# Optimization experiments

Hardware: AMD Instinct MI355X
Metric: run time of the kernel (lower is better)

## Reference

```python
import jax, jax.numpy as jnp
import numpy as np

D = 256; NH = 8; NL = 4; NP = 4; DFF = 2048; HD = D // NH
SHAPES = [(64, 64), (32, 32), (16, 16), (8, 8)]
B = 2; LEN = sum(h * w for h, w in SHAPES)


def setup_inputs() -> dict:
    key = jax.random.key(0)
    ks = jax.random.split(key, 12)
    def w(k, shape, s=0.02):
        return jax.random.normal(k, shape, jnp.float32) * s
    starts = np.cumsum([0] + [h * w for h, w in SHAPES[:-1]])
    return {
        "src": jax.random.normal(ks[0], (B, LEN, D), jnp.float32),
        "pos": jax.random.normal(ks[1], (B, LEN, D), jnp.float32) * 0.1,
        "spatial_shapes": jnp.array(SHAPES, dtype=jnp.int32),
        "level_start_index": jnp.array(starts, dtype=jnp.int32),
        "w_value": w(ks[2], (D, D)), "b_value": jnp.zeros((D,), jnp.float32),
        "w_off": w(ks[3], (D, NH * NL * NP * 2)), "b_off": w(ks[4], (NH * NL * NP * 2,), 0.1),
        "w_attn": w(ks[5], (D, NH * NL * NP)), "b_attn": jnp.zeros((NH * NL * NP,), jnp.float32),
        "w_out": w(ks[6], (D, D)), "b_out": jnp.zeros((D,), jnp.float32),
        "w1": w(ks[7], (D, DFF)), "b1": jnp.zeros((DFF,), jnp.float32),
        "w2": w(ks[8], (DFF, D)), "b2": jnp.zeros((D,), jnp.float32),
        "g1": jnp.ones((D,), jnp.float32), "be1": jnp.zeros((D,), jnp.float32),
        "g2": jnp.ones((D,), jnp.float32), "be2": jnp.zeros((D,), jnp.float32),
    }


def _layer_norm(x, g, b):
    mu = jnp.mean(x, -1, keepdims=True)
    v = jnp.var(x, -1, keepdims=True)
    return (x - mu) * jax.lax.rsqrt(v + 1e-5) * g + b


def _reference_points(shapes):
    # torch.linspace(0.5, H-0.5, H)/H == (arange(H)+0.5)/H
    refs = []
    for H, W in shapes:
        ry = (jnp.arange(H, dtype=jnp.float32) + 0.5) / H
        rx = (jnp.arange(W, dtype=jnp.float32) + 0.5) / W
        yy, xx = jnp.meshgrid(ry, rx, indexing='ij')
        refs.append(jnp.stack([xx.ravel(), yy.ravel()], -1))
    return jnp.concatenate(refs, 0)  # (Len, 2) as (x, y)


def _ms_deform_sample(value, loc, shapes):
    # value: (B, Len, NH, HD); loc: (B, Lq, NH, NL, NP, 2) normalized [0,1]
    # Replicates torch grid_sample(bilinear, padding='zeros', align_corners=False).
    Bn, Lq = loc.shape[0], loc.shape[1]
    P = loc.shape[4]
    start = 0
    outs = []
    for lvl, (H, W) in enumerate(shapes):
        v = value[:, start:start + H * W].transpose(0, 2, 1, 3)  # (B, NH, HW, HD)
        start += H * W
        l = loc[:, :, :, lvl]                      # (B, Lq, NH, P, 2)
        x = l[..., 0] * W - 0.5
        y = l[..., 1] * H - 0.5
        x0 = jnp.floor(x); y0 = jnp.floor(y)
        dx = x - x0; dy = y - y0
        x0i = x0.astype(jnp.int32); y0i = y0.astype(jnp.int32)
        acc = None
        for xi, yi, wgt in ((x0i, y0i, (1 - dx) * (1 - dy)),
                            (x0i + 1, y0i, dx * (1 - dy)),
                            (x0i, y0i + 1, (1 - dx) * dy),
                            (x0i + 1, y0i + 1, dx * dy)):
            valid = ((xi >= 0) & (xi < W) & (yi >= 0) & (yi < H)).astype(value.dtype)
            idx = jnp.clip(yi, 0, H - 1) * W + jnp.clip(xi, 0, W - 1)  # (B, Lq, NH, P)
            idx = idx.transpose(0, 2, 1, 3).reshape(Bn, NH, Lq * P)
            g = jnp.take_along_axis(v, idx[..., None], axis=2).reshape(Bn, NH, Lq, P, HD)
            w = (wgt * valid).transpose(0, 2, 1, 3)[..., None]  # (B, NH, Lq, P, 1)
            acc = g * w if acc is None else acc + g * w
        outs.append(acc)  # (B, NH, Lq, P, HD)
    return jnp.stack(outs, 3)  # (B, NH, Lq, NL, NP, HD)


def _forward(src, pos, w_value, b_value, w_off, b_off, w_attn, b_attn,
             w_out, b_out, w1, b1, w2, b2, g1, be1, g2, be2, shapes):
    Bn, Lq, _ = src.shape
    q = src + pos  # with_pos_embed
    value = (src @ w_value + b_value).reshape(Bn, Lq, NH, HD)
    off = (q @ w_off + b_off).reshape(Bn, Lq, NH, NL, NP, 2)
    attn = jax.nn.softmax((q @ w_attn + b_attn).reshape(Bn, Lq, NH, NL * NP), -1)
    attn = attn.reshape(Bn, Lq, NH, NL, NP)
    ref = _reference_points(shapes)  # (Len, 2)
    normalizer = jnp.array([[w_, h_] for h_, w_ in shapes], jnp.float32)  # (NL, 2) = (W, H)
    loc = ref[None, :, None, None, None, :] + off / normalizer[None, None, None, :, None, :]
    sampled = _ms_deform_sample(value, loc, shapes)  # (B, NH, Lq, NL, NP, HD)
    out = jnp.einsum('bqhlp,bhqlpd->bqhd', attn, sampled).reshape(Bn, Lq, D)
    out = out @ w_out + b_out
    x = _layer_norm(src + out, g1, be1)           # residual + norm1
    ff = jax.nn.relu(x @ w1 + b1) @ w2 + b2       # FFN (dropout=0)
    return _layer_norm(x + ff, g2, be2)           # residual + norm2


def reference(src, pos, spatial_shapes, level_start_index, w_value, b_value,
              w_off, b_off, w_attn, b_attn, w_out, b_out, w1, b1, w2, b2,
              g1, be1, g2, be2):
    shapes = [tuple(int(v) for v in s) for s in np.asarray(spatial_shapes)]
    return _forward(src, pos, w_value, b_value, w_off, b_off, w_attn, b_attn,
                    w_out, b_out, w1, b1, w2, b2, g1, be1, g2, be2, shapes)
```

## Files before the change

kernel.cpp:

```cpp
#include <hip/hip_runtime.h>
#include <math.h>

#define D 256
#define NH 8
#define NL 4
#define NP 4
#define DFF 2048
#define HD 32
#define BB 2
#define LEN 5440
#define MROWS (BB * LEN)

typedef __attribute__((ext_vector_type(8))) short short8;
typedef __attribute__((ext_vector_type(4))) float f32x4;
typedef unsigned int uint32;

__device__ __forceinline__ unsigned short f2bf(float f) {
    uint32 u = __float_as_uint(f);
    u += 0x7FFF + ((u >> 16) & 1);
    return (unsigned short)(u >> 16);
}
__device__ __forceinline__ float bf2f(unsigned short h) {
    return __uint_as_float(((uint32)h) << 16);
}
__device__ __forceinline__ uint32 pack2(float a, float b) {
    return (uint32)f2bf(a) | ((uint32)f2bf(b) << 16);
}

__device__ __forceinline__ void swz85(int b, int ncols, int& row, int& col) {
    const int gsz = ncols << 3;
    const int full = 10 * gsz;
    if (b < full) {
        const int g = b / gsz, idx = b - g * gsz;
        row = (g << 3) + (idx & 7);
        col = idx >> 3;
    } else {
        const int idx = b - full;
        row = 80 + idx % 5;
        col = idx / 5;
    }
}

__global__ void prep(const float* __restrict__ w_value, const float* __restrict__ w_off,
                     const float* __restrict__ w_attn, const float* __restrict__ w_out,
                     const float* __restrict__ w1, const float* __restrict__ w2,
                     const float* __restrict__ b_value, const float* __restrict__ b_off,
                     const float* __restrict__ b_attn,
                     unsigned short* __restrict__ wqvT, unsigned short* __restrict__ woT,
                     unsigned short* __restrict__ w1T, unsigned short* __restrict__ w2T,
                     float* __restrict__ bqv) {
    const int blk = blockIdx.x;
    if (blk >= 1248) {
        for (int i = threadIdx.x; i < 640; i += 256)
            bqv[i] = (i < 256) ? b_value[i] : (i < 512 ? b_off[i - 256] : b_attn[i - 512]);
        return;
    }
    const float* W; unsigned short* WT; int K, N, tid;
    if (blk < 64)       { W = w_value; WT = wqvT;             K = 256;  N = 256;  tid = blk; }
    else if (blk < 128) { W = w_off;   WT = wqvT + 256 * 256; K = 256;  N = 256;  tid = blk - 64; }
    else if (blk < 160) { W = w_attn;  WT = wqvT + 512 * 256; K = 256;  N = 128;  tid = blk - 128; }
    else if (blk < 224) { W = w_out;   WT = woT;              K = 256;  N = 256;  tid = blk - 160; }
    else if (blk < 736) { W = w1;      WT = w1T;              K = 256;  N = 2048; tid = blk - 224; }
    else                { W = w2;      WT = w2T;              K = 2048; N = 256;  tid = blk - 736; }
    const int ntx = N >> 5;
    const int nb = (tid % ntx) * 32, kb = (tid / ntx) * 32;

    __shared__ float tile[32][33];
    const int tx = threadIdx.x & 31, ty = threadIdx.x >> 5;
#pragma unroll
    for (int i = 0; i < 32; i += 8)
        tile[ty + i][tx] = W[(size_t)(kb + ty + i) * N + nb + tx];
    __syncthreads();
#pragma unroll
    for (int i = 0; i < 32; i += 8)
        WT[(size_t)(nb + ty + i) * K + kb + tx] = f2bf(tile[tx][ty + i]);
}

__global__ __launch_bounds__(256) void ffn1_gemm(
        const unsigned short* __restrict__ A,
        const unsigned short* __restrict__ BT, const float* __restrict__ bias,
        unsigned short* __restrict__ Cv, int N, int K, int lda, int ldb) {
    __shared__ unsigned short Ash[2][128][40];
    __shared__ unsigned short Bsh[2][128][40];

    int rowt, colt;
    swz85(blockIdx.x, N >> 7, rowt, colt);
    const int row0 = rowt * 128, col0 = colt * 128;

    const int t = threadIdx.x;
    const int wave = t >> 6, lane = t & 63;
    const int wr = wave >> 1, wc = wave & 1;
    const int lrow = lane & 15, quad = lane >> 4;
    const int srow = t >> 1;
    const int cb = (t & 1) * 16;

    const unsigned short* ap = A + (size_t)(row0 + srow) * lda + cb;
    const unsigned short* bp = BT + (size_t)(col0 + srow) * ldb + cb;

    f32x4 acc[4][4];
#pragma unroll
    for (int i = 0; i < 4; i++)
#pragma unroll
        for (int j = 0; j < 4; j++) acc[i][j] = (f32x4){0.f, 0.f, 0.f, 0.f};

    uint4 ra0 = *(const uint4*)(ap + 0), ra1 = *(const uint4*)(ap + 8);
    uint4 rb0 = *(const uint4*)(bp + 0), rb1 = *(const uint4*)(bp + 8);
    *(uint4*)&Ash[0][srow][cb + 0] = ra0;
    *(uint4*)&Ash[0][srow][cb + 8] = ra1;
    *(uint4*)&Bsh[0][srow][cb + 0] = rb0;
    *(uint4*)&Bsh[0][srow][cb + 8] = rb1;
    if (32 < K) {
        ra0 = *(const uint4*)(ap + 32); ra1 = *(const uint4*)(ap + 40);
        rb0 = *(const uint4*)(bp + 32); rb1 = *(const uint4*)(bp + 40);
    }

    int i = 0;
    for (int kb = 0; kb < K; kb += 32, ++i) {
        __syncthreads();
        if (kb + 32 < K) {
            const int nb = (i + 1) & 1;
            *(uint4*)&Ash[nb][srow][cb + 0] = ra0;
            *(uint4*)&Ash[nb][srow][cb + 8] = ra1;
            *(uint4*)&Bsh[nb][srow][cb + 0] = rb0;
            *(uint4*)&Bsh[nb][srow][cb + 8] = rb1;
            if (kb + 64 < K) {
                ra0 = *(const uint4*)(ap + kb + 64 + 0);
                ra1 = *(const uint4*)(ap + kb + 64 + 8);
                rb0 = *(const uint4*)(bp + kb + 64 + 0);
                rb1 = *(const uint4*)(bp + kb + 64 + 8);
            }
        }
        const int cf = i & 1;
        short8 af[4], bfr[4];
#pragma unroll
        for (int mt = 0; mt < 4; mt++)
            af[mt] = *(const short8*)&Ash[cf][wr * 64 + mt * 16 + lrow][quad * 8];
#pragma unroll
        for (int nt = 0; nt < 4; nt++)
            bfr[nt] = *(const short8*)&Bsh[cf][wc * 64 + nt * 16 + lrow][quad * 8];
#pragma unroll
        for (int mt = 0; mt < 4; mt++)
#pragma unroll
            for (int nt = 0; nt < 4; nt++)
                acc[mt][nt] = __builtin_amdgcn_mfma_f32_16x16x32_bf16(
                    af[mt], bfr[nt], acc[mt][nt], 0, 0, 0);
    }

#pragma unroll
    for (int nt = 0; nt < 4; nt++) {
        const int col = col0 + wc * 64 + nt * 16 + lrow;
        const float bv = bias[col];
#pragma unroll
        for (int mt = 0; mt < 4; mt++) {
            f32x4 a = acc[mt][nt];
#pragma unroll
            for (int r = 0; r < 4; r++) {
                const int row = row0 + wr * 64 + mt * 16 + quad * 4 + r;
                Cv[(size_t)row * N + col] = f2bf(fmaxf(a[r] + bv, 0.f));
            }
        }
    }
}

template <int NZ>
__global__ __launch_bounds__(256) void splitk_gemm(
        const unsigned short* __restrict__ A, const unsigned short* __restrict__ BT,
        unsigned short* __restrict__ part, int KC, int lda, int ldb) {
    __shared__ unsigned short Ash[2][128][40];
    __shared__ unsigned short Bsh[2][128][40];

    int rowt, cc;
    swz85(blockIdx.x, 2 * NZ, rowt, cc);
    const int row0 = rowt * 128;
    const int col0 = (cc & 1) * 128;
    const int z = cc >> 1;
    const int koff = z * KC;
    unsigned short* __restrict__ C = part + (size_t)z * MROWS * 256;

    const int t = threadIdx.x;
    const int wave = t >> 6, lane = t & 63;
    const int wr = wave >> 1, wc = wave & 1;
    const int lrow = lane & 15, quad = lane >> 4;
    const int srow = t >> 1;
    const int cb = (t & 1) * 16;

    const unsigned short* ap = A + (size_t)(row0 + srow) * lda + koff + cb;
    const unsigned short* bp = BT + (size_t)(col0 + srow) * ldb + koff + cb;

    f32x4 acc[4][4];
#pragma unroll
    for (int i = 0; i < 4; i++)
#pragma unroll
        for (int j = 0; j < 4; j++) acc[i][j] = (f32x4){0.f, 0.f, 0.f, 0.f};

    uint4 ra0 = *(const uint4*)(ap + 0), ra1 = *(const uint4*)(ap + 8);
    uint4 rb0 = *(const uint4*)(bp + 0), rb1 = *(const uint4*)(bp + 8);
    *(uint4*)&Ash[0][srow][cb + 0] = ra0;
    *(uint4*)&Ash[0][srow][cb + 8] = ra1;
    *(uint4*)&Bsh[0][srow][cb + 0] = rb0;
    *(uint4*)&Bsh[0][srow][cb + 8] = rb1;
    if (32 < KC) {
        ra0 = *(const uint4*)(ap + 32); ra1 = *(const uint4*)(ap + 40);
        rb0 = *(const uint4*)(bp + 32); rb1 = *(const uint4*)(bp + 40);
    }

    int i = 0;
    for (int kb = 0; kb < KC; kb += 32, ++i) {
        __syncthreads();
        if (kb + 32 < KC) {
            const int nb = (i + 1) & 1;
            *(uint4*)&Ash[nb][srow][cb + 0] = ra0;
            *(uint4*)&Ash[nb][srow][cb + 8] = ra1;
            *(uint4*)&Bsh[nb][srow][cb + 0] = rb0;
            *(uint4*)&Bsh[nb][srow][cb + 8] = rb1;
            if (kb + 64 < KC) {
                ra0 = *(const uint4*)(ap + kb + 64 + 0);
                ra1 = *(const uint4*)(ap + kb + 64 + 8);
                rb0 = *(const uint4*)(bp + kb + 64 + 0);
                rb1 = *(const uint4*)(bp + kb + 64 + 8);
            }
        }
        const int cf = i & 1;
        short8 af[4], bfr[4];
#pragma unroll
        for (int mt = 0; mt < 4; mt++)
            af[mt] = *(const short8*)&Ash[cf][wr * 64 + mt * 16 + lrow][quad * 8];
#pragma unroll
        for (int nt = 0; nt < 4; nt++)
            bfr[nt] = *(const short8*)&Bsh[cf][wc * 64 + nt * 16 + lrow][quad * 8];
#pragma unroll
        for (int mt = 0; mt < 4; mt++)
#pragma unroll
            for (int nt = 0; nt < 4; nt++)
                acc[mt][nt] = __builtin_amdgcn_mfma_f32_16x16x32_bf16(
                    af[mt], bfr[nt], acc[mt][nt], 0, 0, 0);
    }

#pragma unroll
    for (int nt = 0; nt < 4; nt++) {
        const int col = col0 + wc * 64 + nt * 16 + lrow;
#pragma unroll
        for (int mt = 0; mt < 4; mt++) {
            f32x4 a = acc[mt][nt];
#pragma unroll
            for (int r = 0; r < 4; r++) {
                const int row = row0 + wr * 64 + mt * 16 + quad * 4 + r;
                C[(size_t)row * 256 + col] = f2bf(a[r]);
            }
        }
    }
}

__global__ __launch_bounds__(256) void gemm_ln(
        const unsigned short* __restrict__ A, const unsigned short* __restrict__ BT,
        const float* __restrict__ bias, const float* __restrict__ rsd,
        const float* __restrict__ g, const float* __restrict__ be,
        unsigned short* __restrict__ out16, int K) {
    __shared__ __align__(16) unsigned short Ash[32][40];
    __shared__ __align__(16) unsigned short Bsh[256][40];
    __shared__ float red1[4][32], red2[4][32];

    const int row0 = blockIdx.x * 32;
    const int t = threadIdx.x;
    const int wave = t >> 6, lane = t & 63;
    const int lrow = lane & 15, quad = lane >> 4;

    const int ar = t >> 3, ac = (t & 7) * 4;
    const unsigned short* ap = A + (size_t)(row0 + ar) * K + ac;
    const int br = t >> 1, cb = (t & 1) * 16;
    const unsigned short* bp0 = BT + (size_t)br * K + cb;
    const unsigned short* bp1 = BT + (size_t)(128 + br) * K + cb;

    f32x4 acc[2][4];
#pragma unroll
    for (int i = 0; i < 2; i++)
#pragma unroll
        for (int j = 0; j < 4; j++) acc[i][j] = (f32x4){0.f, 0.f, 0.f, 0.f};

    uint2 ra = *(const uint2*)ap;
    uint4 rb00 = *(const uint4*)(bp0 + 0), rb01 = *(const uint4*)(bp0 + 8);
    uint4 rb10 = *(const uint4*)(bp1 + 0), rb11 = *(const uint4*)(bp1 + 8);

    for (int kb = 0; kb < K; kb += 32) {
        __syncthreads();
        *(uint2*)&Ash[ar][ac] = ra;
        *(uint4*)&Bsh[br][cb + 0] = rb00;
        *(uint4*)&Bsh[br][cb + 8] = rb01;
        *(uint4*)&Bsh[128 + br][cb + 0] = rb10;
        *(uint4*)&Bsh[128 + br][cb + 8] = rb11;
        __syncthreads();
        if (kb + 32 < K) {
            ra   = *(const uint2*)(ap + kb + 32);
            rb00 = *(const uint4*)(bp0 + kb + 32 + 0);
            rb01 = *(const uint4*)(bp0 + kb + 32 + 8);
            rb10 = *(const uint4*)(bp1 + kb + 32 + 0);
            rb11 = *(const uint4*)(bp1 + kb + 32 + 8);
        }

        short8 af[2], bfr[4];
#pragma unroll
        for (int mt = 0; mt < 2; mt++)
            af[mt] = *(const short8*)&Ash[mt * 16 + lrow][quad * 8];
#pragma unroll
        for (int nt = 0; nt < 4; nt++)
            bfr[nt] = *(const short8*)&Bsh[wave * 64 + nt * 16 + lrow][quad * 8];
#pragma unroll
        for (int mt = 0; mt < 2; mt++)
#pragma unroll
            for (int nt = 0; nt < 4; nt++)
                acc[mt][nt] = __builtin_amdgcn_mfma_f32_16x16x32_bf16(
                    af[mt], bfr[nt], acc[mt][nt], 0, 0, 0);
    }

    float gv[4], bev[4], bv[4];
#pragma unroll
    for (int nt = 0; nt < 4; nt++) {
        const int col = wave * 64 + nt * 16 + lrow;
        bv[nt] = bias[col];
        gv[nt] = g[col];
        bev[nt] = be[col];
    }

    float v[2][4][4];
#pragma unroll
    for (int mt = 0; mt < 2; mt++)
#pragma unroll
        for (int r = 0; r < 4; r++) {
            const int row = row0 + mt * 16 + quad * 4 + r;
#pragma unroll
            for (int nt = 0; nt < 4; nt++) {
                const int col = wave * 64 + nt * 16 + lrow;
                v[mt][nt][r] = acc[mt][nt][r] + bv[nt] + rsd[(size_t)row * 256 + col];
            }
        }

#pragma unroll
    for (int mt = 0; mt < 2; mt++)
#pragma unroll
        for (int r = 0; r < 4; r++) {
            float s1 = v[mt][0][r] + v[mt][1][r] + v[mt][2][r] + v[mt][3][r];
            float s2 = v[mt][0][r] * v[mt][0][r] + v[mt][1][r] * v[mt][1][r] +
                       v[mt][2][r] * v[mt][2][r] + v[mt][3][r] * v[mt][3][r];
#pragma unroll
            for (int o = 1; o < 16; o <<= 1) {
                s1 += __shfl_xor(s1, o, 16);
                s2 += __shfl_xor(s2, o, 16);
            }
            if (lrow == 0) {
                const int rr = mt * 16 + quad * 4 + r;
                red1[wave][rr] = s1;
                red2[wave][rr] = s2;
            }
        }
    __syncthreads();

#pragma unroll
    for (int mt = 0; mt < 2; mt++)
#pragma unroll
        for (int r = 0; r < 4; r++) {
            const int rr = mt * 16 + quad * 4 + r;
            const float su = red1[0][rr] + red1[1][rr] + red1[2][rr] + red1[3][rr];
            const float sq = red2[0][rr] + red2[1][rr] + red2[2][rr] + red2[3][rr];
            const float mean = su * (1.0f / 256.0f);
            const float var = fmaxf(sq * (1.0f / 256.0f) - mean * mean, 0.f);
            const float rstd = rsqrtf(var + 1e-5f);
            const size_t rowoff = (size_t)(row0 + rr) * 256;
#pragma unroll
            for (int nt = 0; nt < 4; nt++) {
                const int col = wave * 64 + nt * 16 + lrow;
                const float o = (v[mt][nt][r] - mean) * rstd * gv[nt] + bev[nt];
                out16[rowoff + col] = f2bf(o);
            }
        }
}

__global__ __launch_bounds__(256) void qv_gemm(
        const float* __restrict__ src, const float* __restrict__ pos,
        const unsigned short* __restrict__ BT, const float* __restrict__ bias,
        unsigned short* __restrict__ val, unsigned short* __restrict__ qout16) {
    __shared__ unsigned short Ash[2][128][40];
    __shared__ unsigned short Bsh[2][128][40];

    int rowt, colt;
    swz85(blockIdx.x, 5, rowt, colt);
    const int row0 = rowt * 128, col0 = colt * 128;
    const bool addp = (col0 >= 256);

    const int t = threadIdx.x;
    const int wave = t >> 6, lane = t & 63;
    const int wr = wave >> 1, wc = wave & 1;
    const int lrow = lane & 15, quad = lane >> 4;
    const int srow = t >> 1;
    const int cb = (t & 1) * 16;

    const float* ap = src + (size_t)(row0 + srow) * 256 + cb;
    const float* pp = pos + (size_t)(row0 + srow) * 256 + cb;
    const unsigned short* bp = BT + (size_t)(col0 + srow) * 256 + cb;

    f32x4 acc[4][4];
#pragma unroll
    for (int i = 0; i < 4; i++)
#pragma unroll
        for (int j = 0; j < 4; j++) acc[i][j] = (f32x4){0.f, 0.f, 0.f, 0.f};

    float4 fa[4]; float4 fp[4]; uint4 rb0, rb1;
    auto packA = [&](int buf) {
        float4 f0 = fa[0], f1 = fa[1], f2 = fa[2], f3 = fa[3];
        if (addp) {
            f0.x += fp[0].x; f0.y += fp[0].y; f0.z += fp[0].z; f0.w += fp[0].w;
            f1.x += fp[1].x; f1.y += fp[1].y; f1.z += fp[1].z; f1.w += fp[1].w;
            f2.x += fp[2].x; f2.y += fp[2].y; f2.z += fp[2].z; f2.w += fp[2].w;
            f3.x += fp[3].x; f3.y += fp[3].y; f3.z += fp[3].z; f3.w += fp[3].w;
        }
        uint4 u0 = make_uint4(pack2(f0.x, f0.y), pack2(f0.z, f0.w),
                              pack2(f1.x, f1.y), pack2(f1.z, f1.w));
        uint4 u1 = make_uint4(pack2(f2.x, f2.y), pack2(f2.z, f2.w),
                              pack2(f3.x, f3.y), pack2(f3.z, f3.w));
        *(uint4*)&Ash[buf][srow][cb + 0] = u0;
        *(uint4*)&Ash[buf][srow][cb + 8] = u1;
        *(uint4*)&Bsh[buf][srow][cb + 0] = rb0;
        *(uint4*)&Bsh[buf][srow][cb + 8] = rb1;
    };
    auto loadA = [&](int kb) {
#pragma unroll
        for (int j = 0; j < 4; j++) fa[j] = *(const float4*)(ap + kb + 4 * j);
        if (addp) {
#pragma unroll
            for (int j = 0; j < 4; j++) fp[j] = *(const float4*)(pp + kb + 4 * j);
        }
        rb0 = *(const uint4*)(bp + kb + 0);
        rb1 = *(const uint4*)(bp + kb + 8);
    };

    loadA(0);
    packA(0);
    loadA(32);

    int i = 0;
    for (int kb = 0; kb < 256; kb += 32, ++i) {
        __syncthreads();
        if (kb + 32 < 256) {
            packA((i + 1) & 1);
            if (kb + 64 < 256) loadA(kb + 64);
        }
        const int cf = i & 1;
        short8 af[4], bfr[4];
#pragma unroll
        for (int mt = 0; mt < 4; mt++)
            af[mt] = *(const short8*)&Ash[cf][wr * 64 + mt * 16 + lrow][quad * 8];
#pragma unroll
        for (int nt = 0; nt < 4; nt++)
            bfr[nt] = *(const short8*)&Bsh[cf][wc * 64 + nt * 16 + lrow][quad * 8];
#pragma unroll
        for (int mt = 0; mt < 4; mt++)
#pragma unroll
            for (int nt = 0; nt < 4; nt++)
                acc[mt][nt] = __builtin_amdgcn_mfma_f32_16x16x32_bf16(
                    af[mt], bfr[nt], acc[mt][nt], 0, 0, 0);
    }

#pragma unroll
    for (int nt = 0; nt < 4; nt++) {
        const int col = col0 + wc * 64 + nt * 16 + lrow;
        const float bv = bias[col];
#pragma unroll
        for (int mt = 0; mt < 4; mt++) {
            f32x4 a = acc[mt][nt];
#pragma unroll
            for (int r = 0; r < 4; r++) {
                const int row = row0 + wr * 64 + mt * 16 + quad * 4 + r;
                float v = a[r] + bv;
                if (col < 256)
                    val[(size_t)row * 256 + col] = f2bf(v);
                else
                    qout16[(size_t)row * 384 + (col - 256)] = f2bf(v);
            }
        }
    }
}

__global__ void sampler(const unsigned short* __restrict__ val,
                        const unsigned short* __restrict__ qout16,
                        unsigned short* __restrict__ out) {
    __shared__ __align__(16) int   sIdx[2][128][4];
    __shared__ __align__(16) float sW[2][128][4];
    const int t = threadIdx.x;
    const int sub = t >> 7;
    const int tt = t & 127;
    const int bq = blockIdx.x * 2 + sub;
    const int b = bq / LEN, q = bq % LEN;

    {
        const int h = tt >> 4, p = tt & 15;
        const int l = p >> 2;

        float refx, refy;
        if (q < 4096) {
            int rq = q >> 6, cq = q & 63;
            refx = (cq + 0.5f) * (1.0f / 64.0f);
            refy = (rq + 0.5f) * (1.0f / 64.0f);
        } else if (q < 5120) {
            int qq = q - 4096;
            int rq = qq >> 5, cq = qq & 31;
            refx = (cq + 0.5f) * (1.0f / 32.0f);
            refy = (rq + 0.5f) * (1.0f / 32.0f);
        } else if (q < 5376) {
            int qq = q - 5120;
            int rq = qq >> 4, cq = qq & 15;
            refx = (cq + 0.5f) * (1.0f / 16.0f);
            refy = (rq + 0.5f) * (1.0f / 16.0f);
        } else {
            int qq = q - 5376;
            int rq = qq >> 3, cq = qq & 7;
            refx = (cq + 0.5f) * (1.0f / 8.0f);
            refy = (rq + 0.5f) * (1.0f / 8.0f);
        }

        float lv = bf2f(qout16[(size_t)bq * 384 + 256 + tt]);
        float mx = lv;
#pragma unroll
        for (int o = 1; o < 16; o <<= 1) mx = fmaxf(mx, __shfl_xor(mx, o, 16));
        float e = expf(lv - mx);
        float s = e;
#pragma unroll
        for (int o = 1; o < 16; o <<= 1) s += __shfl_xor(s, o, 16);
        const float aw = e / s;

        const uint32 opair = *(const uint32*)&qout16[(size_t)bq * 384 + h * 32 + p * 2];
        const float ox = bf2f((unsigned short)opair);
        const float oy = bf2f((unsigned short)(opair >> 16));

        const int LST[4] = {0, 4096, 5120, 5376};
        const int WW = 64 >> l;
        const float rw = 1.0f / (float)WW;

        float x = (refx + ox * rw) * (float)WW - 0.5f;
        float y = (refy + oy * rw) * (float)WW - 0.5f;
        float x0f = floorf(x), y0f = floorf(y);
        float dx = x - x0f, dy = y - y0f;
        int x0 = (int)x0f, y0 = (int)y0f;

        const int base = (b * LEN + LST[l]) * 256 + h * 32;
        int xs[2] = {x0, x0 + 1}, ys[2] = {y0, y0 + 1};
        float wx[2] = {1.f - dx, dx}, wy[2] = {1.f - dy, dy};
        int ic[4]; float wc4[4];
#pragma unroll
        for (int cy = 0; cy < 2; cy++)
#pragma unroll
            for (int cx = 0; cx < 2; cx++) {
                int xi = xs[cx], yi = ys[cy];
                bool vld = (xi >= 0) && (xi < WW) && (yi >= 0) && (yi < WW);
                int xc = min(max(xi, 0), WW - 1);
                int yc = min(max(yi, 0), WW - 1);
                ic[cy * 2 + cx] = base + (yc * WW + xc) * 256;
                wc4[cy * 2 + cx] = vld ? wx[cx] * wy[cy] * aw : 0.f;
            }
        *(int4*)&sIdx[sub][tt][0] = make_int4(ic[0], ic[1], ic[2], ic[3]);
        *(float4*)&sW[sub][tt][0] = make_float4(wc4[0], wc4[1], wc4[2], wc4[3]);
    }
    __syncthreads();

    const int h = tt >> 4, dp = tt & 15;
    const unsigned short* vald = val + 2 * dp;
    float acc0 = 0.f, acc1 = 0.f;
#pragma unroll 4
    for (int p = 0; p < 16; p++) {
        const int r = h * 16 + p;
        int4 iv = *(const int4*)&sIdx[sub][r][0];
        float4 wv = *(const float4*)&sW[sub][r][0];
        uint32 u0 = *(const uint32*)(vald + iv.x);
        uint32 u1 = *(const uint32*)(vald + iv.y);
        uint32 u2 = *(const uint32*)(vald + iv.z);
        uint32 u3 = *(const uint32*)(vald + iv.w);
        acc0 += bf2f((unsigned short)u0) * wv.x + bf2f((unsigned short)u1) * wv.y +
                bf2f((unsigned short)u2) * wv.z + bf2f((unsigned short)u3) * wv.w;
        acc1 += bf2f((unsigned short)(u0 >> 16)) * wv.x + bf2f((unsigned short)(u1 >> 16)) * wv.y +
                bf2f((unsigned short)(u2 >> 16)) * wv.z + bf2f((unsigned short)(u3 >> 16)) * wv.w;
    }
    *(uint32*)&out[(size_t)bq * D + h * HD + 2 * dp] = pack2(acc0, acc1);
}

__global__ void add_ln4(const unsigned short* __restrict__ part16,
                        const float* __restrict__ bias,
                        const unsigned short* __restrict__ rsd16,
                        const float* __restrict__ g, const float* __restrict__ be,
                        float* __restrict__ out) {
    const int wave = threadIdx.x >> 6, lane = threadIdx.x & 63;
    const int row = blockIdx.x * 4 + wave;
    const int c0 = lane * 4;
    const size_t i = (size_t)row * 256 + c0;

    float v[4];
    {
        ushort4 r = *(const ushort4*)&rsd16[i];
        float4 bv = *(const float4*)&bias[c0];
        v[0] = bf2f(r.x) + bv.x; v[1] = bf2f(r.y) + bv.y;
        v[2] = bf2f(r.z) + bv.z; v[3] = bf2f(r.w) + bv.w;
    }
#pragma unroll
    for (int z = 0; z < 4; z++) {
        ushort4 p = *(const ushort4*)&part16[(size_t)z * MROWS * 256 + i];
        v[0] += bf2f(p.x); v[1] += bf2f(p.y); v[2] += bf2f(p.z); v[3] += bf2f(p.w);
    }
    float s1 = v[0] + v[1] + v[2] + v[3];
    float s2 = v[0] * v[0] + v[1] * v[1] + v[2] * v[2] + v[3] * v[3];
#pragma unroll
    for (int o = 32; o > 0; o >>= 1) {
        s1 += __shfl_xor(s1, o, 64);
        s2 += __shfl_xor(s2, o, 64);
    }
    const float mean = s1 * (1.0f / 256.0f);
    const float var = fmaxf(s2 * (1.0f / 256.0f) - mean * mean, 0.f);
    const float rstd = rsqrtf(var + 1e-5f);

    float4 gv = *(const float4*)&g[c0];
    float4 bev = *(const float4*)&be[c0];
    float4 o4;
    o4.x = (v[0] - mean) * rstd * gv.x + bev.x;
    o4.y = (v[1] - mean) * rstd * gv.y + bev.y;
    o4.z = (v[2] - mean) * rstd * gv.z + bev.z;
    o4.w = (v[3] - mean) * rstd * gv.w + bev.w;
    *(float4*)&out[i] = o4;
}

extern "C" void kernel_launch(void* const* d_in, const int* in_sizes, int n_in,
                              void* d_out, int out_size, void* d_ws, size_t ws_size,
                              hipStream_t stream) {
    const float* src     = (const float*)d_in[0];
    const float* pos     = (const float*)d_in[1];
    const float* w_value = (const float*)d_in[4];
    const float* b_value = (const float*)d_in[5];
    const float* w_off   = (const float*)d_in[6];
    const float* b_off   = (const float*)d_in[7];
    const float* w_attn  = (const float*)d_in[8];
    const float* b_attn  = (const float*)d_in[9];
    const float* w_out   = (const float*)d_in[10];
    const float* b_out   = (const float*)d_in[11];
    const float* w1      = (const float*)d_in[12];
    const float* b1      = (const float*)d_in[13];
    const float* w2      = (const float*)d_in[14];
    const float* b2      = (const float*)d_in[15];
    const float* g1      = (const float*)d_in[16];
    const float* be1     = (const float*)d_in[17];
    const float* g2      = (const float*)d_in[18];
    const float* be2     = (const float*)d_in[19];
    float* out = (float*)d_out;

    size_t off = 0;
    auto alloc = [&](size_t bytes) -> char* {
        char* p = (char*)d_ws + off;
        off += (bytes + 255) & ~(size_t)255;
        return p;
    };
    unsigned short* wqvT = (unsigned short*)alloc((size_t)640 * 256 * 2);
    unsigned short* woT  = (unsigned short*)alloc(256 * 256 * 2);
    unsigned short* w1T  = (unsigned short*)alloc((size_t)2048 * 256 * 2);
    unsigned short* w2T  = (unsigned short*)alloc((size_t)256 * 2048 * 2);
    float* bqv           = (float*)alloc(640 * 4);

    unsigned short* qout = (unsigned short*)alloc((size_t)MROWS * 384 * 2);
    unsigned short* val  = (unsigned short*)alloc((size_t)MROWS * 256 * 2);
    unsigned short* attn = (unsigned short*)alloc((size_t)MROWS * 256 * 2);
    unsigned short* hb   = (unsigned short*)alloc((size_t)MROWS * 2048 * 2);
    unsigned short* xb16 = (unsigned short*)alloc((size_t)MROWS * 256 * 2);
    unsigned short* part = (unsigned short*)alloc((size_t)4 * MROWS * 256 * 2);

    prep<<<1249, 256, 0, stream>>>(w_value, w_off, w_attn, w_out, w1, w2,
                                   b_value, b_off, b_attn, wqvT, woT, w1T, w2T, bqv);

    qv_gemm<<<425, 256, 0, stream>>>(src, pos, wqvT, bqv, val, qout);
    sampler<<<MROWS / 2, 256, 0, stream>>>(val, qout, attn);
    gemm_ln<<<340, 256, 0, stream>>>(attn, woT, b_out, src, g1, be1, xb16, 256);

    ffn1_gemm<<<1360, 256, 0, stream>>>(xb16, w1T, b1, hb, 2048, 256, 256, 256);
    splitk_gemm<4><<<680, 256, 0, stream>>>(hb, w2T, part, 512, 2048, 2048);
    add_ln4<<<MROWS / 4, 256, 0, stream>>>(part, b2, xb16, g2, be2, out);
}
```

Baseline: 205.9 us.

## Stage GEMM tiles with direct global-to-LDS loads and double buffering

```diff
diff --git a/kernel.cpp b/kernel.cpp
--- a/kernel.cpp
+++ b/kernel.cpp
@@ -25,6 +25,12 @@
 }
 __device__ __forceinline__ uint32 pack2(float a, float b) {
     return (uint32)f2bf(a) | ((uint32)f2bf(b) << 16);
+}
+
+__device__ __forceinline__ void gl16(const unsigned short* g, unsigned short* l) {
+    __builtin_amdgcn_global_load_lds(
+        (const __attribute__((address_space(1))) unsigned int*)g,
+        (__attribute__((address_space(3))) unsigned int*)l, 16, 0, 0);
 }
 
 __device__ __forceinline__ void swz85(int b, int ncols, int& row, int& col) {
@@ -80,8 +86,8 @@
         const unsigned short* __restrict__ A,
         const unsigned short* __restrict__ BT, const float* __restrict__ bias,
         unsigned short* __restrict__ Cv, int N, int K, int lda, int ldb) {
-    __shared__ unsigned short Ash[2][128][40];
-    __shared__ unsigned short Bsh[2][128][40];
+    __shared__ unsigned short Ash[2][128][32];
+    __shared__ unsigned short Bsh[2][128][32];
 
     int rowt, colt;
     swz85(blockIdx.x, N >> 7, rowt, colt);
@@ -91,11 +97,10 @@
     const int wave = t >> 6, lane = t & 63;
     const int wr = wave >> 1, wc = wave & 1;
     const int lrow = lane & 15, quad = lane >> 4;
-    const int srow = t >> 1;
-    const int cb = (t & 1) * 16;
-
-    const unsigned short* ap = A + (size_t)(row0 + srow) * lda + cb;
-    const unsigned short* bp = BT + (size_t)(col0 + srow) * ldb + cb;
+    const int sr = lane >> 2, sc = (lane & 3) * 8;
+
+    const unsigned short* Ab = A + (size_t)row0 * lda;
+    const unsigned short* Bb = BT + (size_t)col0 * ldb;
 
     f32x4 acc[4][4];
 #pragma unroll
@@ -103,33 +108,20 @@
 #pragma unroll
         for (int j = 0; j < 4; j++) acc[i][j] = (f32x4){0.f, 0.f, 0.f, 0.f};
 
-    uint4 ra0 = *(const uint4*)(ap + 0), ra1 = *(const uint4*)(ap + 8);
-    uint4 rb0 = *(const uint4*)(bp + 0), rb1 = *(const uint4*)(bp + 8);
-    *(uint4*)&Ash[0][srow][cb + 0] = ra0;
-    *(uint4*)&Ash[0][srow][cb + 8] = ra1;
-    *(uint4*)&Bsh[0][srow][cb + 0] = rb0;
-    *(uint4*)&Bsh[0][srow][cb + 8] = rb1;
-    if (32 < K) {
-        ra0 = *(const uint4*)(ap + 32); ra1 = *(const uint4*)(ap + 40);
-        rb0 = *(const uint4*)(bp + 32); rb1 = *(const uint4*)(bp + 40);
-    }
-
+    auto stage = [&](int buf, int kb) {
+#pragma unroll
+        for (int j = 0; j < 2; j++) {
+            const int r = wave * 32 + j * 16;
+            gl16(Ab + (size_t)(r + sr) * lda + kb + sc, &Ash[buf][r][0]);
+            gl16(Bb + (size_t)(r + sr) * ldb + kb + sc, &Bsh[buf][r][0]);
+        }
+    };
+
+    stage(0, 0);
     int i = 0;
     for (int kb = 0; kb < K; kb += 32, ++i) {
         __syncthreads();
-        if (kb + 32 < K) {
-            const int nb = (i + 1) & 1;
-            *(uint4*)&Ash[nb][srow][cb + 0] = ra0;
-            *(uint4*)&Ash[nb][srow][cb + 8] = ra1;
-            *(uint4*)&Bsh[nb][srow][cb + 0] = rb0;
-            *(uint4*)&Bsh[nb][srow][cb + 8] = rb1;
-            if (kb + 64 < K) {
-                ra0 = *(const uint4*)(ap + kb + 64 + 0);
-                ra1 = *(const uint4*)(ap + kb + 64 + 8);
-                rb0 = *(const uint4*)(bp + kb + 64 + 0);
-                rb1 = *(const uint4*)(bp + kb + 64 + 8);
-            }
-        }
+        if (kb + 32 < K) stage((i + 1) & 1, kb + 32);
         const int cf = i & 1;
         short8 af[4], bfr[4];
 #pragma unroll
@@ -166,8 +158,8 @@
 __global__ __launch_bounds__(256) void splitk_gemm(
         const unsigned short* __restrict__ A, const unsigned short* __restrict__ BT,
         unsigned short* __restrict__ part, int KC, int lda, int ldb) {
-    __shared__ unsigned short Ash[2][128][40];
-    __shared__ unsigned short Bsh[2][128][40];
+    __shared__ unsigned short Ash[2][128][32];
+    __shared__ unsigned short Bsh[2][128][32];
 
     int rowt, cc;
     swz85(blockIdx.x, 2 * NZ, rowt, cc);
@@ -181,11 +173,10 @@
     const int wave = t >> 6, lane = t & 63;
     const int wr = wave >> 1, wc = wave & 1;
     const int lrow = lane & 15, quad = lane >> 4;
-    const int srow = t >> 1;
-    const int cb = (t & 1) * 16;
-
-    const unsigned short* ap = A + (size_t)(row0 + srow) * lda + koff + cb;
-    const unsigned short* bp = BT + (size_t)(col0 + srow) * ldb + koff + cb;
+    const int sr = lane >> 2, sc = (lane & 3) * 8;
+
+    const unsigned short* Ab = A + (size_t)row0 * lda + koff;
+    const unsigned short* Bb = BT + (size_t)col0 * ldb + koff;
 
     f32x4 acc[4][4];
 #pragma unroll
@@ -193,33 +184,20 @@
 #pragma unroll
         for (int j = 0; j < 4; j++) acc[i][j] = (f32x4){0.f, 0.f, 0.f, 0.f};
 
-    uint4 ra0 = *(const uint4*)(ap + 0), ra1 = *(const uint4*)(ap + 8);
-    uint4 rb0 = *(const uint4*)(bp + 0), rb1 = *(const uint4*)(bp + 8);
-    *(uint4*)&Ash[0][srow][cb + 0] = ra0;
-    *(uint4*)&Ash[0][srow][cb + 8] = ra1;
-    *(uint4*)&Bsh[0][srow][cb + 0] = rb0;
-    *(uint4*)&Bsh[0][srow][cb + 8] = rb1;
-    if (32 < KC) {
-        ra0 = *(const uint4*)(ap + 32); ra1 = *(const uint4*)(ap + 40);
-        rb0 = *(const uint4*)(bp + 32); rb1 = *(const uint4*)(bp + 40);
-    }
-
+    auto stage = [&](int buf, int kb) {
+#pragma unroll
+        for (int j = 0; j < 2; j++) {
+            const int r = wave * 32 + j * 16;
+            gl16(Ab + (size_t)(r + sr) * lda + kb + sc, &Ash[buf][r][0]);
+            gl16(Bb + (size_t)(r + sr) * ldb + kb + sc, &Bsh[buf][r][0]);
+        }
+    };
+
+    stage(0, 0);
     int i = 0;
     for (int kb = 0; kb < KC; kb += 32, ++i) {
         __syncthreads();
-        if (kb + 32 < KC) {
-            const int nb = (i + 1) & 1;
-            *(uint4*)&Ash[nb][srow][cb + 0] = ra0;
-            *(uint4*)&Ash[nb][srow][cb + 8] = ra1;
-            *(uint4*)&Bsh[nb][srow][cb + 0] = rb0;
-            *(uint4*)&Bsh[nb][srow][cb + 8] = rb1;
-            if (kb + 64 < KC) {
-                ra0 = *(const uint4*)(ap + kb + 64 + 0);
-                ra1 = *(const uint4*)(ap + kb + 64 + 8);
-                rb0 = *(const uint4*)(bp + kb + 64 + 0);
-                rb1 = *(const uint4*)(bp + kb + 64 + 8);
-            }
-        }
+        if (kb + 32 < KC) stage((i + 1) & 1, kb + 32);
         const int cf = i & 1;
         short8 af[4], bfr[4];
 #pragma unroll
@@ -256,20 +234,15 @@
         const float* __restrict__ bias, const float* __restrict__ rsd,
         const float* __restrict__ g, const float* __restrict__ be,
         unsigned short* __restrict__ out16, int K) {
-    __shared__ __align__(16) unsigned short Ash[32][40];
-    __shared__ __align__(16) unsigned short Bsh[256][40];
+    __shared__ unsigned short Ash[2][32][32];
+    __shared__ unsigned short Bsh[2][256][32];
     __shared__ float red1[4][32], red2[4][32];
 
     const int row0 = blockIdx.x * 32;
     const int t = threadIdx.x;
     const int wave = t >> 6, lane = t & 63;
     const int lrow = lane & 15, quad = lane >> 4;
-
-    const int ar = t >> 3, ac = (t & 7) * 4;
-    const unsigned short* ap = A + (size_t)(row0 + ar) * K + ac;
-    const int br = t >> 1, cb = (t & 1) * 16;
-    const unsigned short* bp0 = BT + (size_t)br * K + cb;
-    const unsigned short* bp1 = BT + (size_t)(128 + br) * K + cb;
+    const int sr = lane >> 2, sc = (lane & 3) * 8;
 
     f32x4 acc[2][4];
 #pragma unroll
@@ -277,33 +250,31 @@
 #pragma unroll
         for (int j = 0; j < 4; j++) acc[i][j] = (f32x4){0.f, 0.f, 0.f, 0.f};
 
-    uint2 ra = *(const uint2*)ap;
-    uint4 rb00 = *(const uint4*)(bp0 + 0), rb01 = *(const uint4*)(bp0 + 8);
-    uint4 rb10 = *(const uint4*)(bp1 + 0), rb11 = *(const uint4*)(bp1 + 8);
-
-    for (int kb = 0; kb < K; kb += 32) {
+    auto stage = [&](int buf, int kb) {
+#pragma unroll
+        for (int j = 0; j < 4; j++) {
+            const int r = wave * 64 + j * 16;
+            gl16(BT + (size_t)(r + sr) * K + kb + sc, &Bsh[buf][r][0]);
+        }
+        if (wave < 2) {
+            const int r = wave * 16;
+            gl16(A + (size_t)(row0 + r + sr) * K + kb + sc, &Ash[buf][r][0]);
+        }
+    };
+
+    stage(0, 0);
+    int it = 0;
+    for (int kb = 0; kb < K; kb += 32, ++it) {
         __syncthreads();
-        *(uint2*)&Ash[ar][ac] = ra;
-        *(uint4*)&Bsh[br][cb + 0] = rb00;
-        *(uint4*)&Bsh[br][cb + 8] = rb01;
-        *(uint4*)&Bsh[128 + br][cb + 0] = rb10;
-        *(uint4*)&Bsh[128 + br][cb + 8] = rb11;
-        __syncthreads();
-        if (kb + 32 < K) {
-            ra   = *(const uint2*)(ap + kb + 32);
-            rb00 = *(const uint4*)(bp0 + kb + 32 + 0);
-            rb01 = *(const uint4*)(bp0 + kb + 32 + 8);
-            rb10 = *(const uint4*)(bp1 + kb + 32 + 0);
-            rb11 = *(const uint4*)(bp1 + kb + 32 + 8);
-        }
-
+        if (kb + 32 < K) stage((it + 1) & 1, kb + 32);
+        const int cf = it & 1;
         short8 af[2], bfr[4];
 #pragma unroll
         for (int mt = 0; mt < 2; mt++)
-            af[mt] = *(const short8*)&Ash[mt * 16 + lrow][quad * 8];
+            af[mt] = *(const short8*)&Ash[cf][mt * 16 + lrow][quad * 8];
 #pragma unroll
         for (int nt = 0; nt < 4; nt++)
-            bfr[nt] = *(const short8*)&Bsh[wave * 64 + nt * 16 + lrow][quad * 8];
+            bfr[nt] = *(const short8*)&Bsh[cf][wave * 64 + nt * 16 + lrow][quad * 8];
 #pragma unroll
         for (int mt = 0; mt < 2; mt++)
 #pragma unroll
@@ -379,7 +350,7 @@
         const unsigned short* __restrict__ BT, const float* __restrict__ bias,
         unsigned short* __restrict__ val, unsigned short* __restrict__ qout16) {
     __shared__ unsigned short Ash[2][128][40];
-    __shared__ unsigned short Bsh[2][128][40];
+    __shared__ unsigned short Bsh[2][128][32];
 
     int rowt, colt;
     swz85(blockIdx.x, 5, rowt, colt);
@@ -392,10 +363,11 @@
     const int lrow = lane & 15, quad = lane >> 4;
     const int srow = t >> 1;
     const int cb = (t & 1) * 16;
+    const int sr = lane >> 2, sc = (lane & 3) * 8;
 
     const float* ap = src + (size_t)(row0 + srow) * 256 + cb;
     const float* pp = pos + (size_t)(row0 + srow) * 256 + cb;
-    const unsigned short* bp = BT + (size_t)(col0 + srow) * 256 + cb;
+    const unsigned short* Bb = BT + (size_t)col0 * 256;
 
     f32x4 acc[4][4];
 #pragma unroll
@@ -403,7 +375,7 @@
 #pragma unroll
         for (int j = 0; j < 4; j++) acc[i][j] = (f32x4){0.f, 0.f, 0.f, 0.f};
 
-    float4 fa[4]; float4 fp[4]; uint4 rb0, rb1;
+    float4 fa[4]; float4 fp[4];
     auto packA = [&](int buf) {
         float4 f0 = fa[0], f1 = fa[1], f2 = fa[2], f3 = fa[3];
         if (addp) {
@@ -418,8 +390,6 @@
                               pack2(f3.x, f3.y), pack2(f3.z, f3.w));
         *(uint4*)&Ash[buf][srow][cb + 0] = u0;
         *(uint4*)&Ash[buf][srow][cb + 8] = u1;
-        *(uint4*)&Bsh[buf][srow][cb + 0] = rb0;
-        *(uint4*)&Bsh[buf][srow][cb + 8] = rb1;
     };
     auto loadA = [&](int kb) {
 #pragma unroll
@@ -428,18 +398,25 @@
 #pragma unroll
             for (int j = 0; j < 4; j++) fp[j] = *(const float4*)(pp + kb + 4 * j);
         }
-        rb0 = *(const uint4*)(bp + kb + 0);
-        rb1 = *(const uint4*)(bp + kb + 8);
+    };
+    auto stageB = [&](int buf, int kb) {
+#pragma unroll
+        for (int j = 0; j < 2; j++) {
+            const int r = wave * 32 + j * 16;
+            gl16(Bb + (size_t)(r + sr) * 256 + kb + sc, &Bsh[buf][r][0]);
+        }
     };
 
     loadA(0);
     packA(0);
+    stageB(0, 0);
     loadA(32);
 
     int i = 0;
     for (int kb = 0; kb < 256; kb += 32, ++i) {
         __syncthreads();
         if (kb + 32 < 256) {
+            stageB((i + 1) & 1, kb + 32);
             packA((i + 1) & 1);
             if (kb + 64 < 256) loadA(kb + 64);
         }
```

Result: no change. 205.4 us (-0.2%).
